# Kernel optimization log

Measured on AMD Instinct MI355X. Metric: run time of the kernel, lower is better.

## Reference

```python
import jax, jax.numpy as jnp
import numpy as np

B, H, W, C_IN, F = 4, 64, 64, 128, 256


def setup_inputs() -> dict:
    key = jax.random.key(0)
    ks = jax.random.split(key, 6)
    return {
        "inputs": jax.random.normal(ks[0], (B, H, W, C_IN), dtype=jnp.float32),
        "W_proj": jax.random.normal(ks[1], (C_IN, F), dtype=jnp.float32) * 0.02,
        "b_proj": jnp.zeros((F,), dtype=jnp.float32),
        "W_q": jax.random.normal(ks[2], (F, F), dtype=jnp.float32) * 0.02,
        "b_q": jnp.zeros((F,), dtype=jnp.float32),
        "W_k": jax.random.normal(ks[3], (F, F), dtype=jnp.float32) * 0.02,
        "b_k": jnp.zeros((F,), dtype=jnp.float32),
        "W_v": jax.random.normal(ks[4], (F, F), dtype=jnp.float32) * 0.02,
        "b_v": jnp.zeros((F,), dtype=jnp.float32),
        "gamma": jax.random.uniform(ks[5], (1,), dtype=jnp.float32),
    }


def reference(inputs, W_proj, b_proj, W_q, b_q, W_k, b_k, W_v, b_v, gamma):
    # 1x1 conv projection (C_in -> filters) since input channels != filters
    x = jnp.einsum("bhwc,cf->bhwf", inputs, W_proj) + b_proj  # [B,H,W,F]
    q = jnp.einsum("bhwf,fg->bhwg", x, W_q) + b_q
    k = jnp.einsum("bhwf,fg->bhwg", x, W_k) + b_k
    v = jnp.einsum("bhwf,fg->bhwg", x, W_v) + b_v
    b, h, w, f = x.shape
    n = h * w
    qr = q.reshape(b, n, f)
    kr = k.reshape(b, n, f)
    vr = v.reshape(b, n, f)
    attn = jax.nn.softmax(jnp.einsum("bnf,bmf->bnm", qr, kr), axis=-1)  # [B,N,N]
    context = jnp.einsum("bnm,bmf->bnf", attn, vr).reshape(b, h, w, f)
    return gamma * context + x
```

## Files before the change

### kernel.cpp

```cpp
#include <hip/hip_runtime.h>
#include <hip/hip_bf16.h>
#include <stdint.h>

typedef __attribute__((ext_vector_type(8))) short short8;
typedef __attribute__((ext_vector_type(4))) float floatx4;
typedef __attribute__((ext_vector_type(16))) float floatx16;

#define DEVI __device__ __forceinline__
#define MFMA16(a, b, c) __builtin_amdgcn_mfma_f32_16x16x32_bf16((a), (b), (c), 0, 0, 0)
#define MFMA32(a, b, c) __builtin_amdgcn_mfma_f32_32x32x16_fp8_fp8((a), (b), (c), 0, 0, 0)

typedef __attribute__((address_space(3))) unsigned int lds_u32;
typedef __attribute__((address_space(1))) const unsigned int glb_u32;
#define GLOAD_LDS16(g, l) __builtin_amdgcn_global_load_lds((glb_u32*)(g), (lds_u32*)(l), 16, 0, 0)

DEVI unsigned short f2bf(float x) {
    union { float f; unsigned int u; } v; v.f = x;
    unsigned int r = v.u + 0x7FFFu + ((v.u >> 16) & 1u);
    return (unsigned short)(r >> 16);
}
DEVI float bf2f(unsigned short h) {
    union { unsigned int u; float f; } v; v.u = ((unsigned int)h) << 16;
    return v.f;
}
DEVI unsigned char f2fp8(float x) {
    int c = __builtin_amdgcn_cvt_pk_fp8_f32(x, x, 0, false);
    return (unsigned char)(c & 0xFF);
}


__global__ void cast_f32_bf16(const float* __restrict__ in, unsigned short* __restrict__ out, int n4) {
    int i = blockIdx.x * blockDim.x + threadIdx.x;
    if (i < n4) {
        float4 v = ((const float4*)in)[i];
        ushort4 o;
        o.x = f2bf(v.x); o.y = f2bf(v.y); o.z = f2bf(v.z); o.w = f2bf(v.w);
        ((ushort4*)out)[i] = o;
    }
}

__global__ void transpose_cast(const float* __restrict__ W, unsigned short* __restrict__ Wt, int K, int N) {
    int idx = blockIdx.x * blockDim.x + threadIdx.x;
    if (idx < K * N) {
        int k = idx / N, n = idx % N;
        Wt[n * K + k] = f2bf(W[idx]);
    }
}

__global__ __launch_bounds__(256) void pack_k8(unsigned char* __restrict__ kb) {
    __shared__ unsigned char T[64][272];
    const int b = blockIdx.y, blk = blockIdx.x;
    unsigned char* base = kb + (size_t)b * 1048576 + (size_t)blk * 16384;
    const int tid = threadIdx.x;
    #pragma unroll
    for (int it = 0; it < 4; ++it) {
        int idx = tid + it * 256;
        int row = idx >> 4, col = (idx & 15) * 16;
        *(int4*)&T[row][col] = *(const int4*)&base[(size_t)row * 256 + col];
    }
    __syncthreads();
    const int w = tid >> 6, lane = tid & 63, l31 = lane & 31, hi = lane >> 5;
    const int tile = w >> 1, sh = (w & 1) * 8;
    #pragma unroll
    for (int i = 0; i < 8; ++i) {
        int s = sh + i;
        long o = *(const long*)&T[tile * 32 + l31][s * 16 + hi * 8];
        *(long*)&base[(size_t)tile * 8192 + (size_t)s * 512 + lane * 8] = o;
    }
}

__global__ __launch_bounds__(256) void pack_v8(unsigned char* __restrict__ vb) {
    __shared__ unsigned char T[64][272];
    const int b = blockIdx.y, blk = blockIdx.x;
    unsigned char* base = vb + (size_t)b * 1048576 + (size_t)blk * 16384;
    const int tid = threadIdx.x;
    #pragma unroll
    for (int it = 0; it < 4; ++it) {
        int idx = tid + it * 256;
        int row = idx >> 4, col = (idx & 15) * 16;
        *(int4*)&T[row][col] = *(const int4*)&base[(size_t)row * 256 + col];
    }
    __syncthreads();
    const int w = tid >> 6, lane = tid & 63, l31 = lane & 31, hi = lane >> 5;
    const int tile = w >> 1, hw = w & 1;
    #pragma unroll
    for (int i = 0; i < 8; ++i) {
        int c = hw * 8 + i;
        int fb = c >> 1, s2 = c & 1;
        union { unsigned char bts[8]; long l; } o;
        #pragma unroll
        for (int j = 0; j < 8; ++j)
            o.bts[j] = T[tile * 32 + s2 * 16 + hi * 8 + j][fb * 32 + l31];
        *(long*)&base[(size_t)tile * 8192 + (size_t)c * 512 + lane * 8] = o.l;
    }
}


template<int K>
__global__ __launch_bounds__(256) void gemm_bias(
    const unsigned short* __restrict__ A,
    const unsigned short* __restrict__ Wt,
    const float* __restrict__ bias,
    unsigned short* __restrict__ Cb,
    int M, int N)
{
    __shared__ unsigned short As[64][136];
    __shared__ unsigned short Bs[64][136];
    const int tid  = threadIdx.x;
    const int w    = tid >> 6;
    const int lane = tid & 63;
    const int quad = lane >> 4;
    const int l15  = lane & 15;
    const int m0 = blockIdx.x * 64;
    const int n0 = blockIdx.y * 64;

    floatx4 acc[4];
    #pragma unroll
    for (int t = 0; t < 4; ++t) acc[t] = (floatx4)0.0f;

    for (int kc = 0; kc < K; kc += 128) {
        __syncthreads();
        #pragma unroll
        for (int idx = tid; idx < 1024; idx += 256) {
            int r = idx >> 4, g = idx & 15;
            *(short8*)&As[r][g * 8] = *(const short8*)&A[(size_t)(m0 + r) * K + kc + g * 8];
            *(short8*)&Bs[r][g * 8] = *(const short8*)&Wt[(size_t)(n0 + r) * K + kc + g * 8];
        }
        __syncthreads();
        #pragma unroll
        for (int s = 0; s < 4; ++s) {
            short8 a = *(const short8*)&As[w * 16 + l15][s * 32 + quad * 8];
            #pragma unroll
            for (int t = 0; t < 4; ++t) {
                short8 bfr = *(const short8*)&Bs[t * 16 + l15][s * 32 + quad * 8];
                acc[t] = MFMA16(a, bfr, acc[t]);
            }
        }
    }

    #pragma unroll
    for (int t = 0; t < 4; ++t) {
        int n = n0 + t * 16 + l15;
        float bs = bias[n];
        #pragma unroll
        for (int r = 0; r < 4; ++r) {
            int m = m0 + w * 16 + quad * 4 + r;
            Cb[(size_t)m * N + n] = f2bf(acc[t][r] + bs);
        }
    }
}

__global__ __launch_bounds__(256) void gemm_qkv(
    const unsigned short* __restrict__ A,
    const unsigned short* __restrict__ Wt0, const unsigned short* __restrict__ Wt1, const unsigned short* __restrict__ Wt2,
    const float* __restrict__ b0, const float* __restrict__ b1, const float* __restrict__ b2,
    unsigned char* __restrict__ C0, unsigned char* __restrict__ C1, unsigned char* __restrict__ C2,
    int M, int N)
{
    const unsigned short* Wt = (blockIdx.z == 0) ? Wt0 : (blockIdx.z == 1) ? Wt1 : Wt2;
    const float* bias        = (blockIdx.z == 0) ? b0  : (blockIdx.z == 1) ? b1  : b2;
    unsigned char* Cb        = (blockIdx.z == 0) ? C0  : (blockIdx.z == 1) ? C1  : C2;

    __shared__ unsigned short As[64][136];
    __shared__ unsigned short Bs[64][136];
    const int tid  = threadIdx.x;
    const int w    = tid >> 6;
    const int lane = tid & 63;
    const int quad = lane >> 4;
    const int l15  = lane & 15;
    const int m0 = blockIdx.x * 64;
    const int n0 = blockIdx.y * 64;

    floatx4 acc[4];
    #pragma unroll
    for (int t = 0; t < 4; ++t) acc[t] = (floatx4)0.0f;

    for (int kc = 0; kc < 256; kc += 128) {
        __syncthreads();
        #pragma unroll
        for (int idx = tid; idx < 1024; idx += 256) {
            int r = idx >> 4, g = idx & 15;
            *(short8*)&As[r][g * 8] = *(const short8*)&A[(size_t)(m0 + r) * 256 + kc + g * 8];
            *(short8*)&Bs[r][g * 8] = *(const short8*)&Wt[(size_t)(n0 + r) * 256 + kc + g * 8];
        }
        __syncthreads();
        #pragma unroll
        for (int s = 0; s < 4; ++s) {
            short8 a = *(const short8*)&As[w * 16 + l15][s * 32 + quad * 8];
            #pragma unroll
            for (int t = 0; t < 4; ++t) {
                short8 bfr = *(const short8*)&Bs[t * 16 + l15][s * 32 + quad * 8];
                acc[t] = MFMA16(a, bfr, acc[t]);
            }
        }
    }

    #pragma unroll
    for (int t = 0; t < 4; ++t) {
        int n = n0 + t * 16 + l15;
        float bs = bias[n];
        #pragma unroll
        for (int r = 0; r < 4; ++r) {
            int m = m0 + w * 16 + quad * 4 + r;
            Cb[(size_t)m * N + n] = f2fp8(acc[t][r] + bs);
        }
    }
}


__global__ __launch_bounds__(512, 2) void flash_attn(
    const unsigned char* __restrict__ qg,
    const unsigned char* __restrict__ kp,
    const unsigned char* __restrict__ vp,
    const unsigned short* __restrict__ xb,
    const float* __restrict__ gamma,
    float* __restrict__ out)
{
    __shared__ __align__(16) unsigned char KV[2][65536];
    float* MbF = (float*)&KV[0][0];
    float* Ml  = MbF + 64 * 264;

    const int tid  = threadIdx.x;
    const int w    = tid >> 6;
    const int lane = tid & 63;
    const int l31  = lane & 31;
    const int hi   = lane >> 5;
    const int kq   = w & 3;
    const int rw   = w >> 2;
    const int blk  = blockIdx.x;
    const int b    = (blk & 7) >> 1;
    const int rt   = (blk >> 3) * 2 + (blk & 1);
    const int row0 = rt * 64 + rw * 32;

    const size_t baseQ = ((size_t)b * 4096 + row0 + l31) * 256 + hi * 8;
    long qf[16];
    #pragma unroll
    for (int s = 0; s < 16; ++s)
        qf[s] = *(const long*)&qg[baseQ + s * 16];

    const long ones8 = 0x3838383838383838L;

    floatx16 ctx[8];
    #pragma unroll
    for (int i = 0; i < 8; ++i) ctx[i] = (floatx16)0.0f;
    floatx16 lacc = (floatx16)0.0f;

    const unsigned char* kb_b = kp + (size_t)b * 1048576;
    const unsigned char* vb_b = vp + (size_t)b * 1048576;

#define FA_STAGE(T, BUF)                                                             \
    {                                                                                \
        _Pragma("unroll")                                                            \
        for (int p = 0; p < 8; ++p) {                                                \
            const int c    = p * 8 + w;                                              \
            const int ckq  = c >> 4;                                                 \
            const int csel = (c >> 3) & 1;                                           \
            const int coff = (c & 7) * 1024;                                         \
            const unsigned char* src = (csel ? vb_b : kb_b)                          \
                + (size_t)ckq * 262144 + (size_t)(T) * 8192 + coff + lane * 16;      \
            GLOAD_LDS16(src, &KV[BUF][ckq * 16384 + csel * 8192 + coff]);            \
        }                                                                            \
    }

    FA_STAGE(0, 0)

    for (int t = 0; t < 32; ++t) {
        const int buf = t & 1;
        __syncthreads();
        if (t < 31) FA_STAGE(t + 1, buf ^ 1)

        const unsigned char* kc = &KV[buf][kq * 16384];
        const unsigned char* vc = &KV[buf][kq * 16384 + 8192];

        floatx16 sa = (floatx16)0.0f, sb = (floatx16)0.0f;
        #pragma unroll
        for (int s = 0; s < 16; s += 2) {
            long k0 = *(const long*)&kc[(size_t)s * 512 + lane * 8];
            long k1 = *(const long*)&kc[(size_t)(s + 1) * 512 + lane * 8];
            sa = MFMA32(k0, qf[s], sa);
            sb = MFMA32(k1, qf[s + 1], sb);
        }

        float e[16];
        #pragma unroll
        for (int r = 0; r < 16; ++r) e[r] = __expf(sa[r] + sb[r]);
        int X0 = __builtin_amdgcn_cvt_pk_fp8_f32(e[0],  e[1],  0,  false);
        X0     = __builtin_amdgcn_cvt_pk_fp8_f32(e[2],  e[3],  X0, true);
        int Y0 = __builtin_amdgcn_cvt_pk_fp8_f32(e[4],  e[5],  0,  false);
        Y0     = __builtin_amdgcn_cvt_pk_fp8_f32(e[6],  e[7],  Y0, true);
        int X1 = __builtin_amdgcn_cvt_pk_fp8_f32(e[8],  e[9],  0,  false);
        X1     = __builtin_amdgcn_cvt_pk_fp8_f32(e[10], e[11], X1, true);
        int Y1 = __builtin_amdgcn_cvt_pk_fp8_f32(e[12], e[13], 0,  false);
        Y1     = __builtin_amdgcn_cvt_pk_fp8_f32(e[14], e[15], Y1, true);
        asm volatile("v_permlane32_swap_b32 %0, %1" : "+v"(X0), "+v"(Y0));
        asm volatile("v_permlane32_swap_b32 %0, %1" : "+v"(X1), "+v"(Y1));
        union { int i2[2]; long l; } u0, u1;
        u0.i2[0] = X0; u0.i2[1] = Y0;
        u1.i2[0] = X1; u1.i2[1] = Y1;
        const long ap0 = u0.l;
        const long ap1 = u1.l;

        lacc = MFMA32(ap0, ones8, lacc);
        lacc = MFMA32(ap1, ones8, lacc);
        #pragma unroll
        for (int fb = 0; fb < 8; ++fb) {
            long v0 = *(const long*)&vc[(size_t)(fb * 2)     * 512 + lane * 8];
            long v1 = *(const long*)&vc[(size_t)(fb * 2 + 1) * 512 + lane * 8];
            ctx[fb] = MFMA32(ap0, v0, ctx[fb]);
            ctx[fb] = MFMA32(ap1, v1, ctx[fb]);
        }
    }
#undef FA_STAGE

    __syncthreads();
    for (int pass = 3; pass >= 0; --pass) {
        if (kq == pass) {
            #pragma unroll
            for (int fb = 0; fb < 8; ++fb) {
                #pragma unroll
                for (int r = 0; r < 16; ++r) {
                    int row = rw * 32 + (r & 3) + 8 * (r >> 2) + 4 * hi;
                    int idx = row * 264 + fb * 32 + l31;
                    float prev = (pass == 3) ? 0.0f : MbF[idx];
                    MbF[idx] = prev + ctx[fb][r];
                }
            }
            if (l31 == 0) {
                #pragma unroll
                for (int r = 0; r < 16; ++r) {
                    int row = rw * 32 + (r & 3) + 8 * (r >> 2) + 4 * hi;
                    float prev = (pass == 3) ? 0.0f : Ml[row];
                    Ml[row] = prev + lacc[r];
                }
            }
        }
        __syncthreads();
    }

    const float g = gamma[0];
    const int row = tid >> 3;
    const int c0  = (tid & 7) * 32;
    const float rl = 1.0f / Ml[row];
    const size_t o = ((size_t)b * 4096 + rt * 64 + row) * 256 + c0;
    #pragma unroll
    for (int j = 0; j < 4; ++j) {
        short8 xv = *(const short8*)&xb[o + j * 8];
        float res[8];
        #pragma unroll
        for (int i = 0; i < 8; ++i)
            res[i] = g * MbF[row * 264 + c0 + j * 8 + i] * rl + bf2f((unsigned short)xv[i]);
        *(float4*)&out[o + j * 8]     = *(float4*)&res[0];
        *(float4*)&out[o + j * 8 + 4] = *(float4*)&res[4];
    }
}


extern "C" void kernel_launch(void* const* d_in, const int* in_sizes, int n_in,
                              void* d_out, int out_size, void* d_ws, size_t ws_size,
                              hipStream_t stream)
{
    const float* inp   = (const float*)d_in[0];
    const float* Wp    = (const float*)d_in[1];
    const float* bp    = (const float*)d_in[2];
    const float* Wq    = (const float*)d_in[3];
    const float* bq    = (const float*)d_in[4];
    const float* Wk    = (const float*)d_in[5];
    const float* bk    = (const float*)d_in[6];
    const float* Wv    = (const float*)d_in[7];
    const float* bv    = (const float*)d_in[8];
    const float* gamma = (const float*)d_in[9];
    float* out = (float*)d_out;

    char* ws = (char*)d_ws;
    unsigned char*  q8    = (unsigned char*)(ws + 0);
    unsigned char*  k8    = (unsigned char*)(ws + 4194304);
    unsigned char*  v8    = (unsigned char*)(ws + 8388608);
    unsigned short* x_b   = (unsigned short*)(ws + 12582912);
    unsigned short* in_b  = (unsigned short*)(ws + 20971520);
    unsigned short* Wt_p  = (unsigned short*)(ws + 25165824);
    unsigned short* Wt_q  = (unsigned short*)(ws + 25231360);
    unsigned short* Wt_k  = (unsigned short*)(ws + 25362432);
    unsigned short* Wt_v  = (unsigned short*)(ws + 25493504);

    cast_f32_bf16<<<2048, 256, 0, stream>>>(inp, in_b, 2097152 / 4);
    transpose_cast<<<128, 256, 0, stream>>>(Wp, Wt_p, 128, 256);
    transpose_cast<<<256, 256, 0, stream>>>(Wq, Wt_q, 256, 256);
    transpose_cast<<<256, 256, 0, stream>>>(Wk, Wt_k, 256, 256);
    transpose_cast<<<256, 256, 0, stream>>>(Wv, Wt_v, 256, 256);

    gemm_bias<128><<<dim3(256, 4), 256, 0, stream>>>(in_b, Wt_p, bp, x_b, 16384, 256);
    gemm_qkv<<<dim3(256, 4, 3), 256, 0, stream>>>(x_b, Wt_q, Wt_k, Wt_v, bq, bk, bv,
                                                  q8, k8, v8, 16384, 256);
    pack_k8<<<dim3(64, 4), 256, 0, stream>>>(k8);
    pack_v8<<<dim3(64, 4), 256, 0, stream>>>(v8);

    flash_attn<<<256, 512, 0, stream>>>(q8, k8, v8, x_b, gamma, out);
}
```

Before: 206.7 us.

## Load packed K/V fragments directly from global memory instead of LDS staging

The K and V packing layouts are changed so each lane's two consecutive 8-byte MFMA fragments sit next to each other as one 16-byte chunk. The flash attention loop drops its double-buffered LDS staging through global_load_lds and per-step barriers. Instead each wave issues 16-byte vector loads straight from global memory into registers. This removes barrier and LDS traffic and cuts shared memory use, which may allow more occupancy. In exchange, global load latency is exposed to the MFMA chain with no explicit prefetch, and the four row-waves sharing a kq re-read the same K/V from cache.

```diff
diff --git a/kernel.cpp b/kernel.cpp
--- a/kernel.cpp
+++ b/kernel.cpp
@@ -5,14 +5,11 @@
 typedef __attribute__((ext_vector_type(8))) short short8;
 typedef __attribute__((ext_vector_type(4))) float floatx4;
 typedef __attribute__((ext_vector_type(16))) float floatx16;
+typedef __attribute__((ext_vector_type(2))) long longx2;
 
 #define DEVI __device__ __forceinline__
 #define MFMA16(a, b, c) __builtin_amdgcn_mfma_f32_16x16x32_bf16((a), (b), (c), 0, 0, 0)
 #define MFMA32(a, b, c) __builtin_amdgcn_mfma_f32_32x32x16_fp8_fp8((a), (b), (c), 0, 0, 0)
-
-typedef __attribute__((address_space(3))) unsigned int lds_u32;
-typedef __attribute__((address_space(1))) const unsigned int glb_u32;
-#define GLOAD_LDS16(g, l) __builtin_amdgcn_global_load_lds((glb_u32*)(g), (lds_u32*)(l), 16, 0, 0)
 
 DEVI unsigned short f2bf(float x) {
     union { float f; unsigned int u; } v; v.f = x;
@@ -65,7 +62,7 @@
     for (int i = 0; i < 8; ++i) {
         int s = sh + i;
         long o = *(const long*)&T[tile * 32 + l31][s * 16 + hi * 8];
-        *(long*)&base[(size_t)tile * 8192 + (size_t)s * 512 + lane * 8] = o;
+        *(long*)&base[(size_t)tile * 8192 + (size_t)(s >> 1) * 1024 + lane * 16 + (s & 1) * 8] = o;
     }
 }
 
@@ -91,7 +88,7 @@
         #pragma unroll
         for (int j = 0; j < 8; ++j)
             o.bts[j] = T[tile * 32 + s2 * 16 + hi * 8 + j][fb * 32 + l31];
-        *(long*)&base[(size_t)tile * 8192 + (size_t)c * 512 + lane * 8] = o.l;
+        *(long*)&base[(size_t)tile * 8192 + (size_t)(c >> 1) * 1024 + lane * 16 + (c & 1) * 8] = o.l;
     }
 }
 
@@ -216,9 +213,8 @@
     const float* __restrict__ gamma,
     float* __restrict__ out)
 {
-    __shared__ __align__(16) unsigned char KV[2][65536];
-    float* MbF = (float*)&KV[0][0];
-    float* Ml  = MbF + 64 * 264;
+    __shared__ __align__(16) float MbF[64 * 264];
+    __shared__ float Ml[64];
 
     const int tid  = threadIdx.x;
     const int w    = tid >> 6;
@@ -245,40 +241,22 @@
     for (int i = 0; i < 8; ++i) ctx[i] = (floatx16)0.0f;
     floatx16 lacc = (floatx16)0.0f;
 
-    const unsigned char* kb_b = kp + (size_t)b * 1048576;
-    const unsigned char* vb_b = vp + (size_t)b * 1048576;
-
-#define FA_STAGE(T, BUF)                                                             \
-    {                                                                                \
-        _Pragma("unroll")                                                            \
-        for (int p = 0; p < 8; ++p) {                                                \
-            const int c    = p * 8 + w;                                              \
-            const int ckq  = c >> 4;                                                 \
-            const int csel = (c >> 3) & 1;                                           \
-            const int coff = (c & 7) * 1024;                                         \
-            const unsigned char* src = (csel ? vb_b : kb_b)                          \
-                + (size_t)ckq * 262144 + (size_t)(T) * 8192 + coff + lane * 16;      \
-            GLOAD_LDS16(src, &KV[BUF][ckq * 16384 + csel * 8192 + coff]);            \
-        }                                                                            \
-    }
-
-    FA_STAGE(0, 0)
+    const unsigned char* kcq = kp + (size_t)b * 1048576 + (size_t)kq * 262144 + lane * 16;
+    const unsigned char* vcq = vp + (size_t)b * 1048576 + (size_t)kq * 262144 + lane * 16;
 
     for (int t = 0; t < 32; ++t) {
-        const int buf = t & 1;
-        __syncthreads();
-        if (t < 31) FA_STAGE(t + 1, buf ^ 1)
-
-        const unsigned char* kc = &KV[buf][kq * 16384];
-        const unsigned char* vc = &KV[buf][kq * 16384 + 8192];
-
+        const unsigned char* kc = kcq + (size_t)t * 8192;
+        const unsigned char* vc = vcq + (size_t)t * 8192;
+
+        longx2 kk[8];
+        #pragma unroll
+        for (int p = 0; p < 8; ++p)
+            kk[p] = *(const longx2*)&kc[p * 1024];
         floatx16 sa = (floatx16)0.0f, sb = (floatx16)0.0f;
         #pragma unroll
-        for (int s = 0; s < 16; s += 2) {
-            long k0 = *(const long*)&kc[(size_t)s * 512 + lane * 8];
-            long k1 = *(const long*)&kc[(size_t)(s + 1) * 512 + lane * 8];
-            sa = MFMA32(k0, qf[s], sa);
-            sb = MFMA32(k1, qf[s + 1], sb);
+        for (int p = 0; p < 8; ++p) {
+            sa = MFMA32(kk[p].x, qf[2 * p],     sa);
+            sb = MFMA32(kk[p].y, qf[2 * p + 1], sb);
         }
 
         float e[16];
@@ -303,14 +281,12 @@
         lacc = MFMA32(ap0, ones8, lacc);
         lacc = MFMA32(ap1, ones8, lacc);
         #pragma unroll
-        for (int fb = 0; fb < 8; ++fb) {
-            long v0 = *(const long*)&vc[(size_t)(fb * 2)     * 512 + lane * 8];
-            long v1 = *(const long*)&vc[(size_t)(fb * 2 + 1) * 512 + lane * 8];
-            ctx[fb] = MFMA32(ap0, v0, ctx[fb]);
-            ctx[fb] = MFMA32(ap1, v1, ctx[fb]);
-        }
-    }
-#undef FA_STAGE
+        for (int p = 0; p < 8; ++p) {
+            longx2 vv = *(const longx2*)&vc[p * 1024];
+            ctx[p] = MFMA32(ap0, vv.x, ctx[p]);
+            ctx[p] = MFMA32(ap1, vv.y, ctx[p]);
+        }
+    }
 
     __syncthreads();
     for (int pass = 3; pass >= 0; --pass) {
```

Measured after the change: 208.6 us. No clear change (+0.9%).
